# Optimization experiments

Measured on AMD Instinct MI355X. Metric: run time of the kernel, lower is better.

Reference implementation:

```python
import jax, jax.numpy as jnp
import numpy as np

N, P, D = 65536, 2048, 512


def setup_inputs() -> dict:
    key = jax.random.key(0)
    k1, k2 = jax.random.split(key)
    embeddings = jax.random.normal(k1, (N, D), dtype=jnp.float32)
    # torch.rand -> uniform [0, 1)
    prototypes = jax.random.uniform(k2, (P, D), dtype=jnp.float32)
    return {"embeddings": embeddings, "prototypes": prototypes}


def reference(embeddings, prototypes):
    # Euclidean distance to prototypes via the quadratic-expansion GEMM trick:
    # torch.norm(embeddings[:,None,:] - prototypes[None,:,:], dim=-1)).
    x_sq = jnp.sum(embeddings * embeddings, axis=-1, keepdims=True)      # [N, 1]
    p_sq = jnp.sum(prototypes * prototypes, axis=-1)[None, :]            # [1, P]
    cross = jnp.einsum("nd,pd->np", embeddings, prototypes)             # [N, P]
    d2 = jnp.maximum(x_sq - 2.0 * cross + p_sq, 0.0)
    dists = jnp.sqrt(d2)
    return -dists  # [N, P]
```

## Files before the change

kernel.cpp:

```cpp
#include <hip/hip_runtime.h>
#include <hip/hip_bf16.h>
#include <cstdint>
#include <math.h>

#define N_EMB   65536
#define N_PROTO 2048
#define DIM     512


typedef __bf16 bf16x8 __attribute__((ext_vector_type(8)));
typedef float  f32x4  __attribute__((ext_vector_type(4)));

__device__ inline bf16x8 cvt8(float4 u, float4 v) {
    bf16x8 r;
    r[0] = (__bf16)u.x; r[1] = (__bf16)u.y; r[2] = (__bf16)u.z; r[3] = (__bf16)u.w;
    r[4] = (__bf16)v.x; r[5] = (__bf16)v.y; r[6] = (__bf16)v.z; r[7] = (__bf16)v.w;
    return r;
}
__device__ inline float dot4(float4 a) { return a.x*a.x + a.y*a.y + a.z*a.z + a.w*a.w; }

__global__ __launch_bounds__(256) void fused_kernel(const float* __restrict__ E,
                                                    const float* __restrict__ Pm,
                                                    float* __restrict__ out) {
    __shared__ __align__(16) __bf16 sA[128 * 32];
    __shared__ __align__(16) __bf16 sB[128 * 32];
    __shared__ __align__(16) float ldsXsq[128];
    __shared__ __align__(16) float ldsPsq[128];

    const int tid   = threadIdx.x;
    const int wave  = tid >> 6, lane = tid & 63;
    const int wm    = wave >> 1, wn = wave & 1;
    const int laneM = lane & 15, laneQ = lane >> 4;

    const int rowBase = blockIdx.y * 128;
    const int colBase = blockIdx.x * 128;

    const int rL   = lane >> 1;
    const int h    = lane & 1;
    const int sRow = wave * 32 + rL;
    const float* gA = E  + (size_t)(rowBase + sRow) * DIM + h * 16;
    const float* gB = Pm + (size_t)(colBase + sRow) * DIM + h * 16;
    __bf16* wA = sA + sRow * 32 + h * 16;
    __bf16* wB = sB + sRow * 32 + h * 16;

    float4 a0 = *(const float4*)(gA + 0), a1 = *(const float4*)(gA + 4);
    float4 a2 = *(const float4*)(gA + 8), a3 = *(const float4*)(gA + 12);
    float4 b0 = *(const float4*)(gB + 0), b1 = *(const float4*)(gB + 4);
    float4 b2 = *(const float4*)(gB + 8), b3 = *(const float4*)(gB + 12);

    float ssqA = 0.0f, ssqB = 0.0f;
    f32x4 acc[4][4] = {};

    #pragma unroll 1
    for (int kt = 0; kt < DIM / 32; ++kt) {
        ssqA += dot4(a0) + dot4(a1) + dot4(a2) + dot4(a3);
        ssqB += dot4(b0) + dot4(b1) + dot4(b2) + dot4(b3);
        *(bf16x8*)(wA)     = cvt8(a0, a1);
        *(bf16x8*)(wA + 8) = cvt8(a2, a3);
        *(bf16x8*)(wB)     = cvt8(b0, b1);
        *(bf16x8*)(wB + 8) = cvt8(b2, b3);
        __syncthreads();

        if (kt != DIM / 32 - 1) {
            const float* nA = gA + (kt + 1) * 32;
            const float* nB = gB + (kt + 1) * 32;
            a0 = *(const float4*)(nA + 0); a1 = *(const float4*)(nA + 4);
            a2 = *(const float4*)(nA + 8); a3 = *(const float4*)(nA + 12);
            b0 = *(const float4*)(nB + 0); b1 = *(const float4*)(nB + 4);
            b2 = *(const float4*)(nB + 8); b3 = *(const float4*)(nB + 12);
        }

        bf16x8 af[4], bfr[4];
        #pragma unroll
        for (int mi = 0; mi < 4; ++mi)
            af[mi] = *(const bf16x8*)(sA + (wm*64 + mi*16 + laneM) * 32 + laneQ * 8);
        #pragma unroll
        for (int ni = 0; ni < 4; ++ni)
            bfr[ni] = *(const bf16x8*)(sB + (wn*64 + ni*16 + laneM) * 32 + laneQ * 8);
        #pragma unroll
        for (int mi = 0; mi < 4; ++mi)
            #pragma unroll
            for (int ni = 0; ni < 4; ++ni)
                acc[mi][ni] = __builtin_amdgcn_mfma_f32_16x16x32_bf16(af[mi], bfr[ni], acc[mi][ni], 0, 0, 0);
        __syncthreads();
    }

    {
        const float vA = ssqA + __shfl_xor(ssqA, 1);
        const float vB = ssqB + __shfl_xor(ssqB, 1);
        if (h == 0) { ldsXsq[sRow] = vA; ldsPsq[sRow] = vB; }
    }
    __syncthreads();

    #pragma unroll
    for (int mi = 0; mi < 4; ++mi) {
        const int rm0 = wm*64 + mi*16 + laneQ*4;
        const float4 xs = *(const float4*)(ldsXsq + rm0);
        #pragma unroll
        for (int ni = 0; ni < 4; ++ni) {
            const int cn = wn*64 + ni*16 + laneM;
            const float pq = ldsPsq[cn];
            float* o = out + (size_t)(rowBase + rm0) * N_PROTO + (colBase + cn);
            const f32x4 c = acc[mi][ni];
            o[0 * N_PROTO] = -sqrtf(fmaxf(xs.x - 2.0f * c[0] + pq, 0.0f));
            o[1 * N_PROTO] = -sqrtf(fmaxf(xs.y - 2.0f * c[1] + pq, 0.0f));
            o[2 * N_PROTO] = -sqrtf(fmaxf(xs.z - 2.0f * c[2] + pq, 0.0f));
            o[3 * N_PROTO] = -sqrtf(fmaxf(xs.w - 2.0f * c[3] + pq, 0.0f));
        }
    }
}

extern "C" void kernel_launch(void* const* d_in, const int* in_sizes, int n_in,
                              void* d_out, int out_size, void* d_ws, size_t ws_size,
                              hipStream_t stream) {
    const float* emb = (const float*)d_in[0];
    const float* pro = (const float*)d_in[1];
    float* out = (float*)d_out;
    (void)d_ws; (void)ws_size; (void)in_sizes; (void)n_in; (void)out_size;

    fused_kernel<<<dim3(N_PROTO / 128, N_EMB / 128), 256, 0, stream>>>(emb, pro, out);
}
```

Baseline: 969.2 us.

## Double-buffer LDS with BK=64, XOR swizzle, block remap, nontemporal stores

Raises the K tile from 32 to 64 and double-buffers the LDS tiles, which halves the barriers per tile and lets the next tile's global loads overlap the MFMA work. An XOR swizzle on the LDS layout is added to avoid bank conflicts. A 1-D grid with an XCD-aware block remap places tiles with shared inputs on the same XCD for L2 reuse. Output writes become nontemporal stores to avoid polluting the cache. The costs are higher register use (16 float4 held per thread) and twice the LDS, which may lower occupancy even with the launch_bounds hint of 2.

```diff
diff --git a/kernel.cpp b/kernel.cpp
--- a/kernel.cpp
+++ b/kernel.cpp
@@ -7,6 +7,10 @@
 #define N_PROTO 2048
 #define DIM     512
 
+#define BM 128
+#define BN 128
+#define BK 64
+#define NT (DIM / BK)
 
 typedef __bf16 bf16x8 __attribute__((ext_vector_type(8)));
 typedef float  f32x4  __attribute__((ext_vector_type(4)));
@@ -19,69 +23,86 @@
 }
 __device__ inline float dot4(float4 a) { return a.x*a.x + a.y*a.y + a.z*a.z + a.w*a.w; }
 
-__global__ __launch_bounds__(256) void fused_kernel(const float* __restrict__ E,
-                                                    const float* __restrict__ Pm,
-                                                    float* __restrict__ out) {
-    __shared__ __align__(16) __bf16 sA[128 * 32];
-    __shared__ __align__(16) __bf16 sB[128 * 32];
-    __shared__ __align__(16) float ldsXsq[128];
-    __shared__ __align__(16) float ldsPsq[128];
+__global__ __launch_bounds__(256, 2) void fused_kernel(const float* __restrict__ E,
+                                                       const float* __restrict__ Pm,
+                                                       float* __restrict__ out) {
+    __shared__ __align__(16) __bf16 sA[2][BM * BK];
+    __shared__ __align__(16) __bf16 sB[2][BN * BK];
+    __shared__ __align__(16) float ldsXsq[BM];
+    __shared__ __align__(16) float ldsPsq[BN];
 
     const int tid   = threadIdx.x;
     const int wave  = tid >> 6, lane = tid & 63;
     const int wm    = wave >> 1, wn = wave & 1;
     const int laneM = lane & 15, laneQ = lane >> 4;
 
-    const int rowBase = blockIdx.y * 128;
-    const int colBase = blockIdx.x * 128;
+    const int bid = blockIdx.x;
+    const int lb  = (bid & 7) * ((N_EMB / BM) * (N_PROTO / BN) / 8) + (bid >> 3);
+    const int rowBase = (lb >> 4) * BM;
+    const int colBase = (lb & 15) * BN;
 
-    const int rL   = lane >> 1;
-    const int h    = lane & 1;
-    const int sRow = wave * 32 + rL;
-    const float* gA = E  + (size_t)(rowBase + sRow) * DIM + h * 16;
-    const float* gB = Pm + (size_t)(colBase + sRow) * DIM + h * 16;
-    __bf16* wA = sA + sRow * 32 + h * 16;
-    __bf16* wB = sB + sRow * 32 + h * 16;
+    const int sRow = tid >> 1;
+    const int h    = tid & 1;
+    const float* gA = E  + (size_t)(rowBase + sRow) * DIM + h * 32;
+    const float* gB = Pm + (size_t)(colBase + sRow) * DIM + h * 32;
 
-    float4 a0 = *(const float4*)(gA + 0), a1 = *(const float4*)(gA + 4);
-    float4 a2 = *(const float4*)(gA + 8), a3 = *(const float4*)(gA + 12);
-    float4 b0 = *(const float4*)(gB + 0), b1 = *(const float4*)(gB + 4);
-    float4 b2 = *(const float4*)(gB + 8), b3 = *(const float4*)(gB + 12);
+    float4 a[8], b[8];
+    float  ssqA = 0.0f, ssqB = 0.0f;
+    f32x4  acc[4][4] = {};
 
-    float ssqA = 0.0f, ssqB = 0.0f;
-    f32x4 acc[4][4] = {};
+    auto loadT = [&](int kt) {
+        const float* pA = gA + kt * BK;
+        const float* pB = gB + kt * BK;
+        #pragma unroll
+        for (int j = 0; j < 8; ++j) a[j] = *(const float4*)(pA + j * 4);
+        #pragma unroll
+        for (int j = 0; j < 8; ++j) b[j] = *(const float4*)(pB + j * 4);
+    };
+    auto stageT = [&](int dst) {
+        #pragma unroll
+        for (int j = 0; j < 8; ++j) ssqA += dot4(a[j]);
+        #pragma unroll
+        for (int j = 0; j < 8; ++j) ssqB += dot4(b[j]);
+        __bf16* wAp = &sA[dst][sRow * BK];
+        __bf16* wBp = &sB[dst][sRow * BK];
+        #pragma unroll
+        for (int j = 0; j < 4; ++j) {
+            const int sl = ((((h << 2) + j) ^ (sRow & 7)) << 3);
+            *(bf16x8*)(wAp + sl) = cvt8(a[2 * j], a[2 * j + 1]);
+            *(bf16x8*)(wBp + sl) = cvt8(b[2 * j], b[2 * j + 1]);
+        }
+    };
+
+    loadT(0);
+    stageT(0);
+    __syncthreads();
 
     #pragma unroll 1
-    for (int kt = 0; kt < DIM / 32; ++kt) {
-        ssqA += dot4(a0) + dot4(a1) + dot4(a2) + dot4(a3);
-        ssqB += dot4(b0) + dot4(b1) + dot4(b2) + dot4(b3);
-        *(bf16x8*)(wA)     = cvt8(a0, a1);
-        *(bf16x8*)(wA + 8) = cvt8(a2, a3);
-        *(bf16x8*)(wB)     = cvt8(b0, b1);
-        *(bf16x8*)(wB + 8) = cvt8(b2, b3);
-        __syncthreads();
+    for (int kt = 0; kt < NT; ++kt) {
+        const int cur = kt & 1;
+        if (kt + 1 < NT) loadT(kt + 1);
 
-        if (kt != DIM / 32 - 1) {
-            const float* nA = gA + (kt + 1) * 32;
-            const float* nB = gB + (kt + 1) * 32;
-            a0 = *(const float4*)(nA + 0); a1 = *(const float4*)(nA + 4);
-            a2 = *(const float4*)(nA + 8); a3 = *(const float4*)(nA + 12);
-            b0 = *(const float4*)(nB + 0); b1 = *(const float4*)(nB + 4);
-            b2 = *(const float4*)(nB + 8); b3 = *(const float4*)(nB + 12);
+        const __bf16* rA = &sA[cur][0];
+        const __bf16* rB = &sB[cur][0];
+        #pragma unroll
+        for (int ks = 0; ks < 2; ++ks) {
+            bf16x8 af[4], bfr[4];
+            #pragma unroll
+            for (int mi = 0; mi < 4; ++mi)
+                af[mi] = *(const bf16x8*)(rA + (wm * 64 + mi * 16 + laneM) * BK
+                                             + ((((ks << 2) + laneQ) ^ (laneM & 7)) << 3));
+            #pragma unroll
+            for (int ni = 0; ni < 4; ++ni)
+                bfr[ni] = *(const bf16x8*)(rB + (wn * 64 + ni * 16 + laneM) * BK
+                                              + ((((ks << 2) + laneQ) ^ (laneM & 7)) << 3));
+            #pragma unroll
+            for (int mi = 0; mi < 4; ++mi)
+                #pragma unroll
+                for (int ni = 0; ni < 4; ++ni)
+                    acc[mi][ni] = __builtin_amdgcn_mfma_f32_16x16x32_bf16(af[mi], bfr[ni], acc[mi][ni], 0, 0, 0);
         }
 
-        bf16x8 af[4], bfr[4];
-        #pragma unroll
-        for (int mi = 0; mi < 4; ++mi)
-            af[mi] = *(const bf16x8*)(sA + (wm*64 + mi*16 + laneM) * 32 + laneQ * 8);
-        #pragma unroll
-        for (int ni = 0; ni < 4; ++ni)
-            bfr[ni] = *(const bf16x8*)(sB + (wn*64 + ni*16 + laneM) * 32 + laneQ * 8);
-        #pragma unroll
-        for (int mi = 0; mi < 4; ++mi)
-            #pragma unroll
-            for (int ni = 0; ni < 4; ++ni)
-                acc[mi][ni] = __builtin_amdgcn_mfma_f32_16x16x32_bf16(af[mi], bfr[ni], acc[mi][ni], 0, 0, 0);
+        if (kt + 1 < NT) stageT(cur ^ 1);
         __syncthreads();
     }
 
@@ -94,18 +115,18 @@
 
     #pragma unroll
     for (int mi = 0; mi < 4; ++mi) {
-        const int rm0 = wm*64 + mi*16 + laneQ*4;
+        const int rm0 = wm * 64 + mi * 16 + laneQ * 4;
         const float4 xs = *(const float4*)(ldsXsq + rm0);
         #pragma unroll
         for (int ni = 0; ni < 4; ++ni) {
-            const int cn = wn*64 + ni*16 + laneM;
+            const int cn = wn * 64 + ni * 16 + laneM;
             const float pq = ldsPsq[cn];
             float* o = out + (size_t)(rowBase + rm0) * N_PROTO + (colBase + cn);
             const f32x4 c = acc[mi][ni];
-            o[0 * N_PROTO] = -sqrtf(fmaxf(xs.x - 2.0f * c[0] + pq, 0.0f));
-            o[1 * N_PROTO] = -sqrtf(fmaxf(xs.y - 2.0f * c[1] + pq, 0.0f));
-            o[2 * N_PROTO] = -sqrtf(fmaxf(xs.z - 2.0f * c[2] + pq, 0.0f));
-            o[3 * N_PROTO] = -sqrtf(fmaxf(xs.w - 2.0f * c[3] + pq, 0.0f));
+            __builtin_nontemporal_store(-sqrtf(fmaxf(xs.x - 2.0f * c[0] + pq, 0.0f)), o + 0 * (size_t)N_PROTO);
+            __builtin_nontemporal_store(-sqrtf(fmaxf(xs.y - 2.0f * c[1] + pq, 0.0f)), o + 1 * (size_t)N_PROTO);
+            __builtin_nontemporal_store(-sqrtf(fmaxf(xs.z - 2.0f * c[2] + pq, 0.0f)), o + 2 * (size_t)N_PROTO);
+            __builtin_nontemporal_store(-sqrtf(fmaxf(xs.w - 2.0f * c[3] + pq, 0.0f)), o + 3 * (size_t)N_PROTO);
         }
     }
 }
@@ -118,5 +139,5 @@
     float* out = (float*)d_out;
     (void)d_ws; (void)ws_size; (void)in_sizes; (void)n_in; (void)out_size;
 
-    fused_kernel<<<dim3(N_PROTO / 128, N_EMB / 128), 256, 0, stream>>>(emb, pro, out);
+    fused_kernel<<<dim3((N_EMB / BM) * (N_PROTO / BN)), 256, 0, stream>>>(emb, pro, out);
 }
```

New measurement: 1.203 ms. 1.24x slower.
